# Kernel tuning notes

Hardware: AMD Instinct MI355X
Metric: run time of the kernel (lower is better)

## Reference

```python
import jax, jax.numpy as jnp
import numpy as np
from jax import lax

B, T, V, E, H, C = 16, 1024, 256, 512, 1024, 256


def lstm_layer(x, h0, c0, Wih, Whh, bih, bhh):
    """Single unidirectional LSTM layer, batch_first. x: (B,T,I). Returns (ys,(h,c)).
    Torch gate order: i, f, g, o. Input projection hoisted out of the scan (one big GEMM)."""
    xg = jnp.einsum('bti,gi->btg', x, Wih) + (bih + bhh)  # (B,T,4H)

    def step(carry, xt):
        h, c = carry
        gates = xt + h @ Whh.T
        i, f, g, o = jnp.split(gates, 4, axis=-1)
        c = jax.nn.sigmoid(f) * c + jax.nn.sigmoid(i) * jnp.tanh(g)
        h = jax.nn.sigmoid(o) * jnp.tanh(c)
        return (h, c), h

    (h, c), ys = lax.scan(step, (h0, c0), jnp.swapaxes(xg, 0, 1))
    return jnp.swapaxes(ys, 0, 1), h, c


def run_stack(emb_tokens, h0s, c0s, layers):
    """layers: list of (Wih, Whh, bih, bhh). h0s/c0s: (L,B,H)."""
    x = emb_tokens
    hs, cs = [], []
    for l, (Wih, Whh, bih, bhh) in enumerate(layers):
        x, h, c = lstm_layer(x, h0s[l], c0s[l], Wih, Whh, bih, bhh)
        hs.append(h)
        cs.append(c)
    return x, jnp.stack(hs), jnp.stack(cs)


def setup_inputs() -> dict:
    key = jax.random.key(0)
    ks = iter(jax.random.split(key, 32))
    s = 1.0 / np.sqrt(H)

    def u(shape):
        return jax.random.uniform(next(ks), shape, jnp.float32, -s, s)

    inp = {"x": jax.random.randint(next(ks), (B, T), 0, V)}
    inp["enc_emb"] = jax.random.normal(next(ks), (V, E), jnp.float32)
    inp["dec_emb"] = jax.random.normal(next(ks), (V, E), jnp.float32)
    for pre in ("enc", "dec"):
        for l in range(2):
            I = E if l == 0 else H
            inp[f"{pre}_Wih{l}"] = u((4 * H, I))
            inp[f"{pre}_Whh{l}"] = u((4 * H, H))
            inp[f"{pre}_bih{l}"] = u((4 * H,))
            inp[f"{pre}_bhh{l}"] = u((4 * H,))
    inp["out_W"] = u((C, H))
    inp["out_b"] = u((C,))
    return inp


def reference(x, enc_emb, dec_emb,
              enc_Wih0, enc_Whh0, enc_bih0, enc_bhh0,
              enc_Wih1, enc_Whh1, enc_bih1, enc_bhh1,
              dec_Wih0, dec_Whh0, dec_bih0, dec_bhh0,
              dec_Wih1, dec_Whh1, dec_bih1, dec_bhh1,
              out_W, out_b):
    enc_layers = [(enc_Wih0, enc_Whh0, enc_bih0, enc_bhh0),
                  (enc_Wih1, enc_Whh1, enc_bih1, enc_bhh1)]
    dec_layers = [(dec_Wih0, dec_Whh0, dec_bih0, dec_bhh0),
                  (dec_Wih1, dec_Whh1, dec_bih1, dec_bhh1)]
    L = len(enc_layers)
    z = jnp.zeros((L, x.shape[0], H), jnp.float32)
    # Encoder (dropout is identity at inference)
    _, h, c = run_stack(enc_emb[x], z, z, enc_layers)
    # Decoder with teacher forcing on the same tokens
    dec_out, _, _ = run_stack(dec_emb[x], h, c, dec_layers)
    logits = dec_out @ out_W.T + out_b  # (B,T,C)
    return jnp.swapaxes(logits, 1, 2)   # (B,C,T)
```

## Files before the change

### kernel.cpp

```cpp
#include <hip/hip_runtime.h>
#include <stdint.h>

#define B_  16
#define T_  1024
#define H_  1024
#define E_  512
#define V_  256
#define C_  256

typedef __bf16 bf16x8 __attribute__((ext_vector_type(8)));
typedef float  f32x4  __attribute__((ext_vector_type(4)));
typedef unsigned int u32x4 __attribute__((ext_vector_type(4)));
typedef unsigned short u16;
typedef unsigned int   u32;
typedef unsigned long long u64;

__device__ __forceinline__ float bf2f(u16 u) {
  union { unsigned int i; float f; } v; v.i = ((unsigned int)u) << 16; return v.f;
}
__device__ __forceinline__ u16 f2bf(float f) {
  union { float f; unsigned int i; } v; v.f = f;
  unsigned int u = v.i;
  return (u16)((u + 0x7fffu + ((u >> 16) & 1u)) >> 16);
}
__device__ __forceinline__ bf16x8 ld_bf8(const u16* p) {
  uint4 v = *(const uint4*)p;
  return __builtin_bit_cast(bf16x8, v);
}
__device__ __forceinline__ float sigm(float x) { return 1.f / (1.f + __expf(-x)); }
__device__ __forceinline__ float tanhfast(float x) {
  return 1.f - 2.f / (__expf(2.f * x) + 1.f);
}

#define LOADQ(d, p) \
  asm volatile("global_load_dwordx4 %0, %1, off sc1" : "=&v"(d) : "v"(p) : "memory")
#define WAITV() do { asm volatile("s_waitcnt vmcnt(0)" ::: "memory"); \
  __builtin_amdgcn_sched_barrier(0); } while (0)

__device__ __forceinline__ u32 tagchk(u32x4 v, u32 tag) {
  return ((v[0] >> 16) ^ tag) | ((v[1] >> 16) ^ tag) |
         ((v[2] >> 16) ^ tag) | ((v[3] >> 16) ^ tag);
}
__device__ __forceinline__ bf16x8 packbf(u32x4 a, u32x4 b) {
  union { u32 w[4]; bf16x8 v; } r;
  r.w[0] = (a[0] & 0xffffu) | (a[1] << 16);
  r.w[1] = (a[2] & 0xffffu) | (a[3] << 16);
  r.w[2] = (b[0] & 0xffffu) | (b[1] << 16);
  r.w[3] = (b[2] & 0xffffu) | (b[3] << 16);
  return r.v;
}

__device__ __forceinline__ void poll4(const u32* p, u32 tag, bf16x8* out) {
  u32x4 a0,b0,a1,b1,a2,b2,a3,b3;
  for (;;) {
    LOADQ(a0,p);      LOADQ(b0,p+4);
    LOADQ(a1,p+32);   LOADQ(b1,p+36);
    LOADQ(a2,p+64);   LOADQ(b2,p+68);
    LOADQ(a3,p+96);   LOADQ(b3,p+100);
    WAITV();
    const u32 bad = tagchk(a0,tag)|tagchk(b0,tag)|tagchk(a1,tag)|tagchk(b1,tag)
                  | tagchk(a2,tag)|tagchk(b2,tag)|tagchk(a3,tag)|tagchk(b3,tag);
    if (!bad) break;
    __builtin_amdgcn_s_sleep(1);
  }
  out[0]=packbf(a0,b0); out[1]=packbf(a1,b1);
  out[2]=packbf(a2,b2); out[3]=packbf(a3,b3);
}

__device__ __forceinline__ void poll8(const u32* xp, u32 xtag,
                                      const u32* hp, u32 htag,
                                      bf16x8* ax, bf16x8* ah) {
  u32x4 xa0,xb0,xa1,xb1,xa2,xb2,xa3,xb3;
  u32x4 ha0,hb0,ha1,hb1,ha2,hb2,ha3,hb3;
  for (;;) {
    LOADQ(xa0,xp);      LOADQ(xb0,xp+4);
    LOADQ(xa1,xp+32);   LOADQ(xb1,xp+36);
    LOADQ(xa2,xp+64);   LOADQ(xb2,xp+68);
    LOADQ(xa3,xp+96);   LOADQ(xb3,xp+100);
    LOADQ(ha0,hp);      LOADQ(hb0,hp+4);
    LOADQ(ha1,hp+32);   LOADQ(hb1,hp+36);
    LOADQ(ha2,hp+64);   LOADQ(hb2,hp+68);
    LOADQ(ha3,hp+96);   LOADQ(hb3,hp+100);
    WAITV();
    const u32 bad =
        tagchk(xa0,xtag)|tagchk(xb0,xtag)|tagchk(xa1,xtag)|tagchk(xb1,xtag)
      | tagchk(xa2,xtag)|tagchk(xb2,xtag)|tagchk(xa3,xtag)|tagchk(xb3,xtag)
      | tagchk(ha0,htag)|tagchk(hb0,htag)|tagchk(ha1,htag)|tagchk(hb1,htag)
      | tagchk(ha2,htag)|tagchk(hb2,htag)|tagchk(ha3,htag)|tagchk(hb3,htag);
    if (!bad) break;
    __builtin_amdgcn_s_sleep(1);
  }
  ax[0]=packbf(xa0,xb0); ax[1]=packbf(xa1,xb1);
  ax[2]=packbf(xa2,xb2); ax[3]=packbf(xa3,xb3);
  ah[0]=packbf(ha0,hb0); ah[1]=packbf(ha1,hb1);
  ah[2]=packbf(ha2,hb2); ah[3]=packbf(ha3,hb3);
}

__device__ __forceinline__ bf16x8 ldw8(const void* W, size_t off, bool f32in) {
  if (f32in) {
    const float* p = (const float*)W + off;
    float4 a = *(const float4*)p;
    float4 b = *(const float4*)(p + 4);
    union { u16 s[8]; bf16x8 v; } r;
    r.s[0]=f2bf(a.x); r.s[1]=f2bf(a.y); r.s[2]=f2bf(a.z); r.s[3]=f2bf(a.w);
    r.s[4]=f2bf(b.x); r.s[5]=f2bf(b.y); r.s[6]=f2bf(b.z); r.s[7]=f2bf(b.w);
    return r.v;
  }
  return ld_bf8((const u16*)W + off);
}
__device__ __forceinline__ float ldb1(const void* p, int i, bool f32in) {
  return f32in ? ((const float*)p)[i] : bf2f(((const u16*)p)[i]);
}

__global__ void probe_k(const u16* __restrict__ s, int* __restrict__ flag) {
  if (threadIdx.x == 0) {
    int cnt = 0;
    for (int i = 0; i < 256; ++i) {
      int e = (s[i] >> 7) & 0xFF;
      if (e >= 124) ++cnt;
    }
    flag[0] = (cnt >= 16) ? 1 : 0;
  }
}

__global__ void cvt_k(const void* __restrict__ src, u16* __restrict__ dst, int n,
                      const int* __restrict__ flagp) {
  int i = blockIdx.x * blockDim.x + threadIdx.x;
  if (i >= n) return;
  if (*flagp) dst[i] = f2bf(((const float*)src)[i]);
  else        dst[i] = ((const u16*)src)[i];
}

struct PersistArgs {
  const int* tok;
  const u16 *eemb, *demb;
  const void *Wih[4], *Whh[4], *bih[4], *bhh[4];
  const u32 *zslot;
  u32 *he0, *he1, *hd0, *hd1;
  u16 *seq;
  u32 *prog;
  const int *dflag;
};

struct PhaseP {
  const void *Wx, *Wh, *bi, *bh;
  const u16* emb;
  const int* tok;
  u32 *r0, *r1;
  const u32 *h0init, *h1init;
  u16* seq;
  u32 *prog;
  bool f32in, init_c;
  int c0, bid, tid;
  u32 gbase;
};

template<int LAYER>
__device__ void run_phase(const PhaseP& q, f32x4* red4, float* gbuf, float* cbuf,
                          float* bbuf) {
  constexpr int KX = LAYER ? 1024 : 512;
  constexpr int NX = KX / 256;
  constexpr int SLOTN = 16 * 1024;
  const int tid = q.tid, w = tid >> 6, l = tid & 63;
  const int rr = l & 15, ksub = (l >> 4) * 8;

  bf16x8 BX[4][NX], BH[4][4];
  #pragma unroll
  for (int g = 0; g < 4; ++g) {
    const size_t row = (size_t)(g * 1024 + q.c0 + rr);
    #pragma unroll
    for (int it = 0; it < NX; ++it)
      BX[g][it] = ldw8(q.Wx, row * KX + w * (KX / 8) + it * 32 + ksub, q.f32in);
    #pragma unroll
    for (int it = 0; it < 4; ++it)
      BH[g][it] = ldw8(q.Wh, row * 1024 + w * 128 + it * 32 + ksub, q.f32in);
  }
  if (tid < 64) {
    const int row = (tid >> 4) * 1024 + q.c0 + (tid & 15);
    bbuf[tid] = ldb1(q.bi, row, q.f32in) + ldb1(q.bh, row, q.f32in);
  }
  if (q.init_c && tid < 64) {
    #pragma unroll
    for (int k = 0; k < 4; ++k) cbuf[k * 64 + tid] = 0.f;
  }
  __syncthreads();

  int tok_cur = LAYER ? 0 : q.tok[rr * T_];
  const int s0 = LAYER ? 1 : 0;
  const int s1 = LAYER ? T_ : T_ - 1;

  for (int s = s0; s <= s1; ++s) {
    bf16x8 ax[NX], ah[4];
    if (LAYER == 0) {
      const u16* xrow = q.emb + (size_t)tok_cur * 512;
      #pragma unroll
      for (int it = 0; it < NX; ++it)
        ax[it] = ld_bf8(xrow + w * (KX / 8) + it * 32 + ksub);
      const u32* hrow = (s == 0) ? (q.h0init + rr * H_)
                                 : (q.r0 + ((s - 1) & 3) * SLOTN + rr * H_);
      poll4(hrow + w * 128 + ksub, q.gbase + (u32)s, ah);
    } else {
      const u32* xrow = q.r0 + ((s - 1) & 3) * SLOTN + rr * H_;
      const u32* hrow = (s == 1) ? (q.h1init + rr * H_)
                                 : (q.r1 + ((s - 2) & 3) * SLOTN + rr * H_);
      poll8(xrow + w * 128 + ksub, q.gbase + (u32)s,
            hrow + w * 128 + ksub, q.gbase + (u32)(s - 1), ax, ah);
    }
    #pragma unroll
    for (int g = 0; g < 4; ++g) {
      f32x4 acc = {0.f, 0.f, 0.f, 0.f};
      #pragma unroll
      for (int it = 0; it < NX; ++it)
        acc = __builtin_amdgcn_mfma_f32_16x16x32_bf16(ax[it], BX[g][it], acc, 0, 0, 0);
      #pragma unroll
      for (int it = 0; it < 4; ++it)
        acc = __builtin_amdgcn_mfma_f32_16x16x32_bf16(ah[it], BH[g][it], acc, 0, 0, 0);
      red4[(w * 4 + g) * 64 + l] = acc;
    }
    if (LAYER == 0)
      tok_cur = q.tok[rr * T_ + ((s + 1 < T_) ? s + 1 : T_ - 1)];
    __syncthreads();
    if (LAYER == 1 && tid == 0)
      __hip_atomic_store(&q.prog[(q.bid & 63) * 16], q.gbase + (u32)s,
                         __ATOMIC_RELAXED, __HIP_MEMORY_SCOPE_AGENT);
    if (tid < 256) {
      const int g = tid >> 6, ll = tid & 63;
      f32x4 ssum = {0.f, 0.f, 0.f, 0.f};
      #pragma unroll
      for (int w8 = 0; w8 < 8; ++w8) ssum += red4[(w8 * 4 + g) * 64 + ll];
      const int n = ll & 15, mg = (ll >> 4) * 4;
      const float bsum = bbuf[g * 16 + n];
      #pragma unroll
      for (int r = 0; r < 4; ++r) gbuf[(g * 16 + n) * 17 + mg + r] = ssum[r] + bsum;
    }
    __syncthreads();
    if (tid < 64) {
      const int m = tid & 15, jg = tid >> 4;
      const u32 stag = LAYER ? (q.gbase + (u32)s) : (q.gbase + (u32)(s + 1));
      u32 wv[4];
      #pragma unroll
      for (int k = 0; k < 4; ++k) {
        const int col = jg * 4 + k;
        const float iv = sigm(gbuf[( 0 + col) * 17 + m]);
        const float fv = sigm(gbuf[(16 + col) * 17 + m]);
        const float gv = tanhfast(gbuf[(32 + col) * 17 + m]);
        const float ov = sigm(gbuf[(48 + col) * 17 + m]);
        const float cn = fv * cbuf[k * 64 + tid] + iv * gv;
        cbuf[k * 64 + tid] = cn;
        wv[k] = (stag << 16) | (u32)f2bf(ov * tanhfast(cn));
      }
      if (LAYER == 0 && s >= 4) {
        const u32 need = q.gbase + (u32)(s - 3);
        while (__hip_atomic_load(&q.prog[tid * 16], __ATOMIC_RELAXED,
                                 __HIP_MEMORY_SCOPE_AGENT) < need)
          __builtin_amdgcn_s_sleep(2);
      }
      u32* outs = LAYER ? (q.r1 + ((s - 1) & 3) * SLOTN)
                        : (q.r0 + (s & 3) * SLOTN);
      u64* dst = (u64*)(outs + (size_t)m * H_ + q.c0 + jg * 4);
      __hip_atomic_store(dst,     (u64)wv[0] | ((u64)wv[1] << 32),
                         __ATOMIC_RELAXED, __HIP_MEMORY_SCOPE_AGENT);
      __hip_atomic_store(dst + 1, (u64)wv[2] | ((u64)wv[3] << 32),
                         __ATOMIC_RELAXED, __HIP_MEMORY_SCOPE_AGENT);
      if (q.seq) {
        union { u16 s4[4]; u64 q8; } hp;
        #pragma unroll
        for (int k = 0; k < 4; ++k) hp.s4[k] = (u16)(wv[k] & 0xffffu);
        const int t = s - 1;
        *(u64*)(q.seq + ((size_t)m * T_ + t) * H_ + q.c0 + jg * 4) = hp.q8;
      }
    }
  }
}

__global__ __launch_bounds__(512, 2) void persist_k(PersistArgs P) {
  __shared__ f32x4 red4[32 * 64];
  __shared__ float gbuf[64 * 17];
  __shared__ float cbuf[4 * 64];
  __shared__ float bbuf[64];
  const int bid = blockIdx.x, tid = threadIdx.x;
  const int layer = bid >> 6;
  const int c0 = (bid & 63) * 16;
  const bool f32in = (*P.dflag != 0);
  constexpr int SLOTN = 16 * 1024;

  for (int ph = 0; ph < 2; ++ph) {
    PhaseP q;
    const int wi = ph * 2 + layer;
    q.Wx = P.Wih[wi]; q.Wh = P.Whh[wi]; q.bi = P.bih[wi]; q.bh = P.bhh[wi];
    q.emb = ph ? P.demb : P.eemb;
    q.tok = P.tok;
    q.r0 = ph ? P.hd0 : P.he0;
    q.r1 = ph ? P.hd1 : P.he1;
    q.h0init = ph ? (P.he0 + 3 * SLOTN) : P.zslot;
    q.h1init = ph ? (P.he1 + 3 * SLOTN) : P.zslot;
    q.seq = (ph == 1 && layer == 1) ? P.seq : nullptr;
    q.prog = P.prog;
    q.f32in = f32in; q.init_c = (ph == 0);
    q.c0 = c0; q.bid = bid; q.tid = tid;
    q.gbase = ph ? 1024u : 0u;
    if (layer) run_phase<1>(q, red4, gbuf, cbuf, bbuf);
    else       run_phase<0>(q, red4, gbuf, cbuf, bbuf);
  }
}

__global__ __launch_bounds__(256) void logits_k(const u16* __restrict__ A,
                                                const u16* __restrict__ W,
                                                const u16* __restrict__ bias,
                                                void* __restrict__ out,
                                                const int* __restrict__ dflag) {
  const int wid  = blockIdx.x * 4 + (threadIdx.x >> 6);
  const int mt   = wid >> 4;
  const int nt   = wid & 15;
  const int lane = threadIdx.x & 63;
  const int l15  = lane & 15;
  const int quad = lane >> 4;
  const int ko   = quad * 8;
  const u16* arow = A + (size_t)(mt * 16 + l15) * H_;
  const u16* brow = W + (size_t)(nt * 16 + l15) * H_;
  f32x4 acc = {0.f,0.f,0.f,0.f};
  #pragma unroll 4
  for (int kk = 0; kk < H_; kk += 32) {
    acc = __builtin_amdgcn_mfma_f32_16x16x32_bf16(ld_bf8(arow + kk + ko),
                                                  ld_bf8(brow + kk + ko), acc, 0, 0, 0);
  }
  const int c  = nt * 16 + l15;
  const float bv = bf2f(bias[c]);
  const int f32out = *dflag;
  #pragma unroll
  for (int r = 0; r < 4; ++r) {
    const int m = mt * 16 + quad * 4 + r;
    const int b = m >> 10, t = m & 1023;
    const size_t idx = ((size_t)b * C_ + c) * T_ + t;
    const float v = acc[r] + bv;
    if (f32out) ((float*)out)[idx] = v;
    else        ((u16*)out)[idx]   = f2bf(v);
  }
}

extern "C" void kernel_launch(void* const* d_in, const int* in_sizes, int n_in,
                              void* d_out, int out_size, void* d_ws, size_t ws_size,
                              hipStream_t stream) {
  (void)in_sizes; (void)n_in; (void)out_size; (void)ws_size;

  const int* x = (const int*)d_in[0];

  char* ws = (char*)d_ws;
  u32* prog   = (u32*)ws;
  int* dflag  = (int*)(ws + 16384);
  u32* zslot  = (u32*)(ws + 16640);
  u32* rings  = (u32*)(ws + 82176);
  char* base  = ws + 1130752;
  size_t ob = 0;
  u16* p_eemb = (u16*)(base + ob); ob += (size_t)V_ * E_ * 2;
  u16* p_demb = (u16*)(base + ob); ob += (size_t)V_ * E_ * 2;
  u16* p_outW = (u16*)(base + ob); ob += (size_t)C_ * H_ * 2;
  u16* p_outb = (u16*)(base + ob); ob += 512;
  u16* seq    = (u16*)(base + ob); ob += (size_t)B_ * T_ * H_ * 2;
  const size_t RING = 4 * (size_t)16 * 1024;

  hipMemsetAsync(ws, 0, 1130752, stream);

  probe_k<<<1, 64, 0, stream>>>((const u16*)d_in[5], dflag);

  cvt_k<<<(V_ * E_ + 255) / 256, 256, 0, stream>>>(d_in[1], p_eemb, V_ * E_, dflag);
  cvt_k<<<(V_ * E_ + 255) / 256, 256, 0, stream>>>(d_in[2], p_demb, V_ * E_, dflag);
  cvt_k<<<(C_ * H_ + 255) / 256, 256, 0, stream>>>(d_in[19], p_outW, C_ * H_, dflag);
  cvt_k<<<1, 256, 0, stream>>>(d_in[20], p_outb, C_, dflag);

  PersistArgs P;
  P.tok = x; P.eemb = p_eemb; P.demb = p_demb;
  for (int l = 0; l < 4; ++l) {
    P.Wih[l] = d_in[3 + 4 * l + 0];
    P.Whh[l] = d_in[3 + 4 * l + 1];
    P.bih[l] = d_in[3 + 4 * l + 2];
    P.bhh[l] = d_in[3 + 4 * l + 3];
  }
  P.zslot = zslot;
  P.he0 = rings + 0 * RING;
  P.he1 = rings + 1 * RING;
  P.hd0 = rings + 2 * RING;
  P.hd1 = rings + 3 * RING;
  P.seq = seq; P.prog = prog; P.dflag = dflag;

  persist_k<<<128, 512, 0, stream>>>(P);

  logits_k<<<4096, 256, 0, stream>>>(seq, p_outW, p_outb, d_out, dflag);
}
```

Baseline: 16.99 ms.

## Deepen hidden-state ring to 8 slots and lighten spin polling

The ring buffer that carries h between layer-0 and layer-1 blocks grows from 4 to 8 slots, which loosens the back-pressure wait so layer 0 can run further ahead of layer 1. The progress-counter load is issued early, right after the poll, so that in the common case the later spin wait is skipped. Failed polls now re-check with cheap single-dword tag probes before redoing the full vector load. The workspace layout and memset grow to hold the larger rings. The risk is extra memory traffic and a weaker check: the probe samples only some of the words, but the outer loop still re-verifies every tag before proceeding.

```diff
diff --git a/kernel.cpp b/kernel.cpp
--- a/kernel.cpp
+++ b/kernel.cpp
@@ -34,6 +34,8 @@
 
 #define LOADQ(d, p) \
   asm volatile("global_load_dwordx4 %0, %1, off sc1" : "=&v"(d) : "v"(p) : "memory")
+#define LOADD(d, p) \
+  asm volatile("global_load_dword %0, %1, off sc1" : "=v"(d) : "v"(p) : "memory")
 #define WAITV() do { asm volatile("s_waitcnt vmcnt(0)" ::: "memory"); \
   __builtin_amdgcn_sched_barrier(0); } while (0)
 
@@ -61,7 +63,16 @@
     const u32 bad = tagchk(a0,tag)|tagchk(b0,tag)|tagchk(a1,tag)|tagchk(b1,tag)
                   | tagchk(a2,tag)|tagchk(b2,tag)|tagchk(a3,tag)|tagchk(b3,tag);
     if (!bad) break;
-    __builtin_amdgcn_s_sleep(1);
+    for (;;) {
+      __builtin_amdgcn_s_sleep(2);
+      u32 c0,c1,c2,c3,c4,c5,c6,c7;
+      LOADD(c0,p);    LOADD(c1,p+7);   LOADD(c2,p+32);  LOADD(c3,p+39);
+      LOADD(c4,p+64); LOADD(c5,p+71);  LOADD(c6,p+96);  LOADD(c7,p+103);
+      WAITV();
+      const u32 pb = ((c0>>16)^tag)|((c1>>16)^tag)|((c2>>16)^tag)|((c3>>16)^tag)
+                   | ((c4>>16)^tag)|((c5>>16)^tag)|((c6>>16)^tag)|((c7>>16)^tag);
+      if (!pb) break;
+    }
   }
   out[0]=packbf(a0,b0); out[1]=packbf(a1,b1);
   out[2]=packbf(a2,b2); out[3]=packbf(a3,b3);
@@ -88,7 +99,21 @@
       | tagchk(ha0,htag)|tagchk(hb0,htag)|tagchk(ha1,htag)|tagchk(hb1,htag)
       | tagchk(ha2,htag)|tagchk(hb2,htag)|tagchk(ha3,htag)|tagchk(hb3,htag);
     if (!bad) break;
-    __builtin_amdgcn_s_sleep(1);
+    for (;;) {
+      __builtin_amdgcn_s_sleep(2);
+      u32 c0,c1,c2,c3,c4,c5,c6,c7,d0,d1,d2,d3,d4,d5,d6,d7;
+      LOADD(c0,xp);    LOADD(c1,xp+7);  LOADD(c2,xp+32); LOADD(c3,xp+39);
+      LOADD(c4,xp+64); LOADD(c5,xp+71); LOADD(c6,xp+96); LOADD(c7,xp+103);
+      LOADD(d0,hp);    LOADD(d1,hp+7);  LOADD(d2,hp+32); LOADD(d3,hp+39);
+      LOADD(d4,hp+64); LOADD(d5,hp+71); LOADD(d6,hp+96); LOADD(d7,hp+103);
+      WAITV();
+      const u32 pb =
+          ((c0>>16)^xtag)|((c1>>16)^xtag)|((c2>>16)^xtag)|((c3>>16)^xtag)
+        | ((c4>>16)^xtag)|((c5>>16)^xtag)|((c6>>16)^xtag)|((c7>>16)^xtag)
+        | ((d0>>16)^htag)|((d1>>16)^htag)|((d2>>16)^htag)|((d3>>16)^htag)
+        | ((d4>>16)^htag)|((d5>>16)^htag)|((d6>>16)^htag)|((d7>>16)^htag);
+      if (!pb) break;
+    }
   }
   ax[0]=packbf(xa0,xb0); ax[1]=packbf(xa1,xb1);
   ax[2]=packbf(xa2,xb2); ax[3]=packbf(xa3,xb3);
@@ -191,20 +216,22 @@
 
   for (int s = s0; s <= s1; ++s) {
     bf16x8 ax[NX], ah[4];
+    u32 pval = 0;
     if (LAYER == 0) {
       const u16* xrow = q.emb + (size_t)tok_cur * 512;
       #pragma unroll
       for (int it = 0; it < NX; ++it)
         ax[it] = ld_bf8(xrow + w * (KX / 8) + it * 32 + ksub);
-      const u32* hrow = (s == 0) ? (q.h0init + rr * H_)
-                                 : (q.r0 + ((s - 1) & 3) * SLOTN + rr * H_);
-      poll4(hrow + w * 128 + ksub, q.gbase + (u32)s, ah);
+      const u32* hslot = (s == 0) ? q.h0init : (q.r0 + ((s - 1) & 7) * SLOTN);
+      poll4(hslot + rr * H_ + w * 128 + ksub, q.gbase + (u32)s, ah);
+      if (s >= 8 && tid < 64)
+        pval = __hip_atomic_load(&q.prog[tid * 16], __ATOMIC_RELAXED,
+                                 __HIP_MEMORY_SCOPE_AGENT);
     } else {
-      const u32* xrow = q.r0 + ((s - 1) & 3) * SLOTN + rr * H_;
-      const u32* hrow = (s == 1) ? (q.h1init + rr * H_)
-                                 : (q.r1 + ((s - 2) & 3) * SLOTN + rr * H_);
-      poll8(xrow + w * 128 + ksub, q.gbase + (u32)s,
-            hrow + w * 128 + ksub, q.gbase + (u32)(s - 1), ax, ah);
+      const u32* xslot = q.r0 + ((s - 1) & 7) * SLOTN;
+      const u32* hslot = (s == 1) ? q.h1init : (q.r1 + ((s - 2) & 7) * SLOTN);
+      poll8(xslot + rr * H_ + w * 128 + ksub, q.gbase + (u32)s,
+            hslot + rr * H_ + w * 128 + ksub, q.gbase + (u32)(s - 1), ax, ah);
     }
     #pragma unroll
     for (int g = 0; g < 4; ++g) {
@@ -249,14 +276,16 @@
         cbuf[k * 64 + tid] = cn;
         wv[k] = (stag << 16) | (u32)f2bf(ov * tanhfast(cn));
       }
-      if (LAYER == 0 && s >= 4) {
-        const u32 need = q.gbase + (u32)(s - 3);
-        while (__hip_atomic_load(&q.prog[tid * 16], __ATOMIC_RELAXED,
-                                 __HIP_MEMORY_SCOPE_AGENT) < need)
-          __builtin_amdgcn_s_sleep(2);
+      if (LAYER == 0 && s >= 8) {
+        const u32 need = q.gbase + (u32)(s - 7);
+        if (pval < need) {
+          while (__hip_atomic_load(&q.prog[tid * 16], __ATOMIC_RELAXED,
+                                   __HIP_MEMORY_SCOPE_AGENT) < need)
+            __builtin_amdgcn_s_sleep(2);
+        }
       }
-      u32* outs = LAYER ? (q.r1 + ((s - 1) & 3) * SLOTN)
-                        : (q.r0 + (s & 3) * SLOTN);
+      u32* outs = LAYER ? (q.r1 + ((s - 1) & 7) * SLOTN)
+                        : (q.r0 + (s & 7) * SLOTN);
       u64* dst = (u64*)(outs + (size_t)m * H_ + q.c0 + jg * 4);
       __hip_atomic_store(dst,     (u64)wv[0] | ((u64)wv[1] << 32),
                          __ATOMIC_RELAXED, __HIP_MEMORY_SCOPE_AGENT);
@@ -292,8 +321,8 @@
     q.tok = P.tok;
     q.r0 = ph ? P.hd0 : P.he0;
     q.r1 = ph ? P.hd1 : P.he1;
-    q.h0init = ph ? (P.he0 + 3 * SLOTN) : P.zslot;
-    q.h1init = ph ? (P.he1 + 3 * SLOTN) : P.zslot;
+    q.h0init = ph ? (P.he0 + 7 * SLOTN) : P.zslot;
+    q.h1init = ph ? (P.he1 + 7 * SLOTN) : P.zslot;
     q.seq = (ph == 1 && layer == 1) ? P.seq : nullptr;
     q.prog = P.prog;
     q.f32in = f32in; q.init_c = (ph == 0);
@@ -350,16 +379,16 @@
   int* dflag  = (int*)(ws + 16384);
   u32* zslot  = (u32*)(ws + 16640);
   u32* rings  = (u32*)(ws + 82176);
-  char* base  = ws + 1130752;
+  char* base  = ws + 2179328;
   size_t ob = 0;
   u16* p_eemb = (u16*)(base + ob); ob += (size_t)V_ * E_ * 2;
   u16* p_demb = (u16*)(base + ob); ob += (size_t)V_ * E_ * 2;
   u16* p_outW = (u16*)(base + ob); ob += (size_t)C_ * H_ * 2;
   u16* p_outb = (u16*)(base + ob); ob += 512;
   u16* seq    = (u16*)(base + ob); ob += (size_t)B_ * T_ * H_ * 2;
-  const size_t RING = 4 * (size_t)16 * 1024;
-
-  hipMemsetAsync(ws, 0, 1130752, stream);
+  const size_t RING = 8 * (size_t)16 * 1024;
+
+  hipMemsetAsync(ws, 0, 2179328, stream);
 
   probe_k<<<1, 64, 0, stream>>>((const u16*)d_in[5], dflag);
 
```

Measured after the change: 25.86 ms. +52.2%, slower.
